# Optimization experiments

Hardware: AMD Instinct MI355X
Metric: run time of the kernel (lower is better)

The kernel has to match this reference:

```python
import jax, jax.numpy as jnp
import numpy as np

B, N, K, C_IN, C_OUT = 4, 8192, 32, 64, 64
MID = (C_OUT + C_IN) // 2  # 64, since C_IN is even
GROUPS = 8
EPS = 1e-5
SLOPE = 0.1


def group_norm(x, gamma, beta, groups=GROUPS, eps=EPS):
    # x: [b, ..., C], normalize per-sample over all spatial dims and group channels
    b = x.shape[0]
    C = x.shape[-1]
    xr = x.reshape(b, -1, groups, C // groups)
    mean = xr.mean(axis=(1, 3), keepdims=True)
    var = xr.var(axis=(1, 3), keepdims=True)
    xn = ((xr - mean) / jnp.sqrt(var + eps)).reshape(x.shape)
    return xn * gamma + beta


def lrelu(x):
    return jnp.where(x >= 0, x, SLOPE * x)


def setup_inputs() -> dict:
    key = jax.random.key(0)
    ks = jax.random.split(key, 10)
    signal = jax.random.normal(ks[0], (B, N, C_IN), dtype=jnp.float32)
    edges = jax.random.randint(ks[1], (B * N * K,), 0, B * N, dtype=jnp.int64)
    edge_feats = jax.random.normal(ks[2], (B * N * K, 3), dtype=jnp.float32)
    W1 = jax.random.normal(ks[3], (MID, C_IN + 3), dtype=jnp.float32) * 0.1
    W2 = jax.random.normal(ks[4], (C_OUT, MID), dtype=jnp.float32) * 0.1
    W3 = jax.random.normal(ks[5], (C_OUT, C_OUT), dtype=jnp.float32) * 0.1
    return {
        "signal": signal, "edges": edges, "edge_feats": edge_feats,
        "W1": W1, "g1": jnp.ones((MID,), jnp.float32), "b1": jnp.zeros((MID,), jnp.float32),
        "W2": W2, "g2": jnp.ones((C_OUT,), jnp.float32), "b2": jnp.zeros((C_OUT,), jnp.float32),
        "W3": W3, "g3": jnp.ones((C_OUT,), jnp.float32), "b3": jnp.zeros((C_OUT,), jnp.float32),
    }


def reference(signal, edges, edge_feats, W1, g1, b1, W2, g2, b2, W3, g3, b3):
    b, n, c = signal.shape
    k = edges.shape[0] // (b * n)
    flat = signal.reshape(b * n, c)
    # gather neighbor features and take relative difference: [b*n, k, c]
    ef = flat[edges].reshape(b * n, k, c) - flat[:, None, :]
    # concat relative coordinates -> [b, n, k, c+3]
    x = jnp.concatenate([ef, edge_feats.reshape(b * n, k, 3)], axis=-1)
    x = x.reshape(b, n, k, c + 3)
    # 1x1 conv (fc1) + GN + lrelu
    x = jnp.einsum('bnkc,mc->bnkm', x, W1)
    x = lrelu(group_norm(x, g1, b1))
    # max-pool over neighbors -> [b, n, mid]
    x = jnp.max(x, axis=2)
    # fc2 + GN + lrelu
    x = jnp.einsum('bnm,om->bno', x, W2)
    x = lrelu(group_norm(x, g2, b2))
    # fc3 + GN + lrelu
    x = jnp.einsum('bno,po->bnp', x, W3)
    x = lrelu(group_norm(x, g3, b3))
    return x  # [b, n, nb_feat_out]
```

## Files before the change

kernel.cpp:

```cpp
#include <hip/hip_runtime.h>

#define NB    4
#define NPB   8192
#define NPTS  (NB*NPB)
#define KNB   32
#define CH    64
#define W1C   67
#define GRPS  8
#define EPSV  1e-5f
#define SLOPEV 0.1f

typedef float f32x2 __attribute__((ext_vector_type(2)));
typedef float f32x4 __attribute__((ext_vector_type(4)));
typedef short bf16x8 __attribute__((ext_vector_type(8)));
typedef unsigned short u16;
typedef u16 u16x4 __attribute__((ext_vector_type(4)));
typedef u16 u16x8 __attribute__((ext_vector_type(8)));

#define WS_STATS1 0
#define WS_STATS2 64
#define WS_STATS3 128
#define WS_FLAG   192
#define WS_YB     256
#define WS_MX     (WS_YB + NPTS*CH/2)
#define WS_MN     (WS_MX + NPTS*CH/2)

#define LDP 72

__device__ __forceinline__ u16 f2bf(float f) {
    unsigned u = __float_as_uint(f);
    u += 0x7fff + ((u >> 16) & 1);
    return (u16)(u >> 16);
}
__device__ __forceinline__ float bf2f(u16 h) {
    return __uint_as_float(((unsigned)h) << 16);
}

template<int MODE>
__global__ __launch_bounds__(256) void k_mm(
    const void* __restrict__ X0,
    const void* __restrict__ X1,
    const float* __restrict__ Wg,
    const float* __restrict__ statsIn, float invcnt,
    const float* __restrict__ gm, const float* __restrict__ bt,
    void* __restrict__ Out,
    float* __restrict__ statsOut,
    const int* __restrict__ e_i32, int* __restrict__ flag)
{
    __shared__ u16 Al[64*LDP];
    __shared__ u16 Wl[64*LDP];
    __shared__ float affA[64], affB[64];
    __shared__ float lacc[16];
    __shared__ int sfnd[4];
    int tid = threadIdx.x;
    int pbase = blockIdx.x * 64;
    int b = pbase >> 13;

    if (MODE == 0 && blockIdx.x == 0) {
        if (tid < 192) statsOut[tid] = 0.f;
        int found = 0;
        #pragma unroll
        for (int i = 0; i < 16; ++i) {
            int idx = ((tid << 4) + i) * 2 + 1;
            found |= (e_i32[idx] != 0);
        }
        unsigned long long bl = __ballot(found);
        if ((tid & 63) == 0) sfnd[tid >> 6] = (bl != 0ull) ? 1 : 0;
    }
    if (MODE != 0) {
        if (tid < 64) {
            int g = tid >> 3;
            float sv = statsIn[b*16 + g*2 + 0];
            float qv = statsIn[b*16 + g*2 + 1];
            float mean = sv * invcnt;
            float var  = fmaf(-mean, mean, qv * invcnt);
            float rstd = rsqrtf(var + EPSV);
            float a = gm[tid] * rstd;
            affA[tid] = a;
            affB[tid] = fmaf(-mean, a, bt[tid]);
        }
    }
    if (tid < 16) lacc[tid] = 0.f;
    __syncthreads();
    if (MODE == 0 && blockIdx.x == 0 && tid == 0)
        *flag = sfnd[0] | sfnd[1] | sfnd[2] | sfnd[3];

    {
        const int wstride = (MODE == 0) ? W1C : 64;
        #pragma unroll
        for (int i = 0; i < 16; ++i) {
            int e = tid + 256*i;
            int o = e >> 6, m = e & 63;
            Wl[o*LDP + m] = f2bf(Wg[o*wstride + m]);
        }
    }
    #pragma unroll
    for (int it = 0; it < 4; ++it) {
        int fi = it*1024 + tid*4;
        int p = fi >> 6;
        int m = fi & 63;
        float xv[4];
        if (MODE == 1) {
            u16x4 vx = *(const u16x4*)&((const u16*)X0)[(pbase+p)*64 + m];
            u16x4 vn = *(const u16x4*)&((const u16*)X1)[(pbase+p)*64 + m];
            #pragma unroll
            for (int j = 0; j < 4; ++j) {
                float a = affA[m+j];
                float x = (a < 0.f) ? bf2f(vn[j]) : bf2f(vx[j]);
                float z = fmaf(a, x, affB[m+j]);
                xv[j] = (z >= 0.f) ? z : SLOPEV * z;
            }
        } else if (MODE == 2) {
            u16x4 vh = *(const u16x4*)&((const u16*)X0)[(pbase+p)*64 + m];
            #pragma unroll
            for (int j = 0; j < 4; ++j) {
                float z = fmaf(affA[m+j], bf2f(vh[j]), affB[m+j]);
                xv[j] = (z >= 0.f) ? z : SLOPEV * z;
            }
        } else {
            f32x4 vx = *(const f32x4*)&((const float*)X0)[(pbase+p)*64 + m];
            #pragma unroll
            for (int j = 0; j < 4; ++j) xv[j] = vx[j];
        }
        #pragma unroll
        for (int j = 0; j < 4; ++j)
            Al[p*LDP + m + j] = f2bf(xv[j]);
    }
    __syncthreads();

    int l = tid & 63, w = tid >> 6;
    int lr = l & 15;
    int lk = l >> 4;
    bf16x8 af[2], bw[4][2];
    #pragma unroll
    for (int kh = 0; kh < 2; ++kh)
        af[kh] = *(const bf16x8*)&Al[(w*16 + lr)*LDP + kh*32 + lk*8];
    #pragma unroll
    for (int ot = 0; ot < 4; ++ot)
        #pragma unroll
        for (int kh = 0; kh < 2; ++kh)
            bw[ot][kh] = *(const bf16x8*)&Wl[(ot*16 + lr)*LDP + kh*32 + lk*8];

    f32x4 acc[4];
    #pragma unroll
    for (int ot = 0; ot < 4; ++ot) {
        f32x4 c = {0.f, 0.f, 0.f, 0.f};
        c = __builtin_amdgcn_mfma_f32_16x16x32_bf16(af[0], bw[ot][0], c, 0, 0, 0);
        c = __builtin_amdgcn_mfma_f32_16x16x32_bf16(af[1], bw[ot][1], c, 0, 0, 0);
        acc[ot] = c;
    }

    #pragma unroll
    for (int ot = 0; ot < 4; ++ot)
        #pragma unroll
        for (int r = 0; r < 4; ++r) {
            int p = pbase + w*16 + lk*4 + r;
            int o = ot*16 + lr;
            ((u16*)Out)[p*64 + o] = f2bf(acc[ot][r]);
        }

    if (MODE != 0) {
        #pragma unroll
        for (int ot = 0; ot < 4; ++ot) {
            float s = 0.f, ss = 0.f;
            #pragma unroll
            for (int r = 0; r < 4; ++r) {
                float v = acc[ot][r];
                s += v;
                ss = fmaf(v, v, ss);
            }
            s += __shfl_xor(s, 16, 64);  ss += __shfl_xor(ss, 16, 64);
            s += __shfl_xor(s, 32, 64);  ss += __shfl_xor(ss, 32, 64);
            s += __shfl_xor(s, 1, 64);   ss += __shfl_xor(ss, 1, 64);
            s += __shfl_xor(s, 2, 64);   ss += __shfl_xor(ss, 2, 64);
            s += __shfl_xor(s, 4, 64);   ss += __shfl_xor(ss, 4, 64);
            if ((l & 7) == 0 && l < 16) {
                int g = ot*2 + (l >> 3);
                atomicAdd(&lacc[g*2 + 0], s);
                atomicAdd(&lacc[g*2 + 1], ss);
            }
        }
        __syncthreads();
        if (tid < 16)
            atomicAdd(&statsOut[b*16 + tid], lacc[tid]);
    }
}

#define PPB_E 32
#define SEDS  (KNB*4 + 4)
__global__ __launch_bounds__(256) void k_edge(const u16* __restrict__ Yb,
    const void* __restrict__ edg, const float* __restrict__ ef,
    const float* __restrict__ W1, const int* __restrict__ flag,
    u16* __restrict__ Mx, u16* __restrict__ Mn, float* __restrict__ stats1)
{
    __shared__ float sed[PPB_E*SEDS];
    __shared__ float lacc[16];
    int tid = threadIdx.x;
    if (tid < 16) lacc[tid] = 0.f;

    {
        bool is32 = (*flag != 0);
        const int*       e32 = (const int*)edg;
        const long long* e64 = (const long long*)edg;
        int ebase = blockIdx.x * (PPB_E*KNB);
        #pragma unroll
        for (int i = 0; i < 4; ++i) {
            int idx = tid + i*256;
            int gi  = ebase + idx;
            int e   = is32 ? __builtin_nontemporal_load(e32 + gi)
                           : (int)__builtin_nontemporal_load(e64 + gi);
            int pt = idx >> 5, k = idx & 31;
            float* d = &sed[pt*SEDS + k*4];
            d[0] = __builtin_nontemporal_load(ef + gi*3 + 0);
            d[1] = __builtin_nontemporal_load(ef + gi*3 + 1);
            d[2] = __builtin_nontemporal_load(ef + gi*3 + 2);
            d[3] = __int_as_float(e << 7);
        }
    }

    int lane = tid & 63, wv = tid >> 6;
    int il = lane & 7;
    int g8 = lane >> 3;
    int lpt = wv*8 + g8;
    int p = blockIdx.x * PPB_E + lpt;

    f32x2 w0[4], w1[4], w2[4], yp[4], mx[4], mn[4];
    #pragma unroll
    for (int jj = 0; jj < 4; ++jj) {
        int ch = il*8 + jj*2;
        w0[jj] = (f32x2){W1[ch*W1C + 64], W1[(ch+1)*W1C + 64]};
        w1[jj] = (f32x2){W1[ch*W1C + 65], W1[(ch+1)*W1C + 65]};
        w2[jj] = (f32x2){W1[ch*W1C + 66], W1[(ch+1)*W1C + 66]};
    }
    u16x8 yh = *(const u16x8*)&Yb[p*64 + il*8];
    #pragma unroll
    for (int jj = 0; jj < 4; ++jj) {
        yp[jj] = (f32x2){bf2f(yh[jj*2]), bf2f(yh[jj*2+1])};
        mx[jj] = (f32x2){-3.4e38f, -3.4e38f};
        mn[jj] = (f32x2){ 3.4e38f,  3.4e38f};
    }
    f32x2 s2 = {0.f, 0.f}, ss2 = {0.f, 0.f};
    __syncthreads();

    const char* Ybase = (const char*)Yb + il*16;
    const float* sp = &sed[lpt*SEDS];
    #pragma unroll 8
    for (int k = 0; k < KNB; ++k) {
        f32x4 m4 = *(const f32x4*)(sp + k*4);
        u16x8 q = *(const u16x8*)(Ybase + __float_as_int(m4[3]));
        f32x2 c0v = m4[0], c1v = m4[1], c2v = m4[2];
        #pragma unroll
        for (int jj = 0; jj < 4; ++jj) {
            f32x2 qq = {bf2f(q[jj*2]), bf2f(q[jj*2+1])};
            f32x2 t = qq - yp[jj];
            t = __builtin_elementwise_fma(c0v, w0[jj], t);
            t = __builtin_elementwise_fma(c1v, w1[jj], t);
            t = __builtin_elementwise_fma(c2v, w2[jj], t);
            mx[jj] = __builtin_elementwise_max(mx[jj], t);
            mn[jj] = __builtin_elementwise_min(mn[jj], t);
            s2 += t;
            ss2 = __builtin_elementwise_fma(t, t, ss2);
        }
    }

    u16x8 hx, hn;
    #pragma unroll
    for (int jj = 0; jj < 4; ++jj) {
        hx[jj*2] = f2bf(mx[jj].x); hx[jj*2+1] = f2bf(mx[jj].y);
        hn[jj*2] = f2bf(mn[jj].x); hn[jj*2+1] = f2bf(mn[jj].y);
    }
    __builtin_nontemporal_store(hx, (u16x8*)(Mx + p*64 + il*8));
    __builtin_nontemporal_store(hn, (u16x8*)(Mn + p*64 + il*8));

    float s  = s2.x + s2.y;
    float ss = ss2.x + ss2.y;
    s += __shfl_xor(s,  8, 64);  ss += __shfl_xor(ss,  8, 64);
    s += __shfl_xor(s, 16, 64);  ss += __shfl_xor(ss, 16, 64);
    s += __shfl_xor(s, 32, 64);  ss += __shfl_xor(ss, 32, 64);
    if (lane < 8) {
        atomicAdd(&lacc[lane*2 + 0], s);
        atomicAdd(&lacc[lane*2 + 1], ss);
    }
    __syncthreads();
    if (tid < 16) {
        int b = (blockIdx.x * PPB_E) / NPB;
        atomicAdd(&stats1[b*16 + tid], lacc[tid]);
    }
}

__global__ __launch_bounds__(256) void k_out(const u16* __restrict__ Vpre,
    const float* __restrict__ stats, float invcnt,
    const float* __restrict__ gm, const float* __restrict__ bt,
    float* __restrict__ out)
{
    int idx = blockIdx.x * blockDim.x + threadIdx.x;
    int p  = idx >> 4;
    int m0 = (idx & 15) << 2;
    int b  = p >> 13;
    int g  = m0 >> 3;
    float sv = stats[b*16 + g*2 + 0];
    float qv = stats[b*16 + g*2 + 1];
    float mean = sv * invcnt;
    float var  = fmaf(-mean, mean, qv * invcnt);
    float rstd = rsqrtf(var + EPSV);
    u16x4 v = *(const u16x4*)&Vpre[idx*4];
    float r[4];
    #pragma unroll
    for (int j = 0; j < 4; ++j) {
        float aa = gm[m0+j] * rstd;
        float z  = fmaf(aa, bf2f(v[j]) - mean, bt[m0+j]);
        r[j] = (z >= 0.f) ? z : SLOPEV * z;
    }
    f32x4 o4 = {r[0], r[1], r[2], r[3]};
    *(f32x4*)&out[idx*4] = o4;
}

extern "C" void kernel_launch(void* const* d_in, const int* in_sizes, int n_in,
                              void* d_out, int out_size, void* d_ws, size_t ws_size,
                              hipStream_t stream)
{
    const float* sig = (const float*)d_in[0];
    const void*  edg = d_in[1];
    const float* ef  = (const float*)d_in[2];
    const float* W1  = (const float*)d_in[3];
    const float* g1  = (const float*)d_in[4];
    const float* b1  = (const float*)d_in[5];
    const float* W2  = (const float*)d_in[6];
    const float* g2  = (const float*)d_in[7];
    const float* b2  = (const float*)d_in[8];
    const float* W3  = (const float*)d_in[9];
    const float* g3  = (const float*)d_in[10];
    const float* b3  = (const float*)d_in[11];
    float* out = (float*)d_out;
    float* ws  = (float*)d_ws;
    u16*   yb  = (u16*)(ws + WS_YB);
    u16*   mxb = (u16*)(ws + WS_MX);
    u16*   mnb = (u16*)(ws + WS_MN);

    k_mm<0><<<NPTS/64, 256, 0, stream>>>(sig, nullptr, W1, nullptr, 0.f,
                                          nullptr, nullptr, yb, ws,
                                          (const int*)edg, (int*)(ws + WS_FLAG));
    k_edge<<<NPTS/PPB_E, 256, 0, stream>>>(yb, edg, ef, W1,
                                           (const int*)(ws + WS_FLAG),
                                           mxb, mnb, ws + WS_STATS1);
    k_mm<1><<<NPTS/64, 256, 0, stream>>>(mxb, mnb, W2,
                                          ws + WS_STATS1, 1.f/(float)(NPB*KNB*8),
                                          g1, b1, yb, ws + WS_STATS2,
                                          nullptr, nullptr);
    k_mm<2><<<NPTS/64, 256, 0, stream>>>(yb, nullptr, W3,
                                          ws + WS_STATS2, 1.f/(float)(NPB*8),
                                          g2, b2, mxb, ws + WS_STATS3,
                                          nullptr, nullptr);
    k_out<<<(NPTS*CH/4)/256, 256, 0, stream>>>(mxb, ws + WS_STATS3,
                                         1.f/(float)(NPB*8), g3, b3, out);
}
```

Measured before the change: 57.58 us.

## Load MFMA A-fragments directly from global and enlarge edge blocks

```diff
diff --git a/kernel.cpp b/kernel.cpp
--- a/kernel.cpp
+++ b/kernel.cpp
@@ -6,7 +6,6 @@
 #define KNB   32
 #define CH    64
 #define W1C   67
-#define GRPS  8
 #define EPSV  1e-5f
 #define SLOPEV 0.1f
 
@@ -20,12 +19,13 @@
 #define WS_STATS1 0
 #define WS_STATS2 64
 #define WS_STATS3 128
-#define WS_FLAG   192
 #define WS_YB     256
 #define WS_MX     (WS_YB + NPTS*CH/2)
 #define WS_MN     (WS_MX + NPTS*CH/2)
 
-#define LDP 72
+#define LDPW 68
+#define SEDS (KNB*4 + 4)
+#define EPB  64
 
 __device__ __forceinline__ u16 f2bf(float f) {
     unsigned u = __float_as_uint(f);
@@ -36,37 +36,32 @@
     return __uint_as_float(((unsigned)h) << 16);
 }
 
+__device__ __forceinline__ bool probe_is32(const int* e_i32, int tid) {
+    int found = 0;
+    #pragma unroll
+    for (int i = 0; i < 8; ++i)
+        found |= (e_i32[(tid*8 + i)*2 + 1] != 0);
+    return (__ballot(found) != 0ull);
+}
+
 template<int MODE>
 __global__ __launch_bounds__(256) void k_mm(
-    const void* __restrict__ X0,
-    const void* __restrict__ X1,
+    const void* __restrict__ X0, const void* __restrict__ X1,
     const float* __restrict__ Wg,
     const float* __restrict__ statsIn, float invcnt,
     const float* __restrict__ gm, const float* __restrict__ bt,
-    void* __restrict__ Out,
-    float* __restrict__ statsOut,
-    const int* __restrict__ e_i32, int* __restrict__ flag)
+    u16* __restrict__ Out, float* __restrict__ statsOut,
+    float* __restrict__ zeroStats)
 {
-    __shared__ u16 Al[64*LDP];
-    __shared__ u16 Wl[64*LDP];
-    __shared__ float affA[64], affB[64];
+    __shared__ u16 Wl[64*LDPW];
+    __shared__ __align__(16) float affA[64];
+    __shared__ __align__(16) float affB[64];
     __shared__ float lacc[16];
-    __shared__ int sfnd[4];
     int tid = threadIdx.x;
     int pbase = blockIdx.x * 64;
     int b = pbase >> 13;
 
-    if (MODE == 0 && blockIdx.x == 0) {
-        if (tid < 192) statsOut[tid] = 0.f;
-        int found = 0;
-        #pragma unroll
-        for (int i = 0; i < 16; ++i) {
-            int idx = ((tid << 4) + i) * 2 + 1;
-            found |= (e_i32[idx] != 0);
-        }
-        unsigned long long bl = __ballot(found);
-        if ((tid & 63) == 0) sfnd[tid >> 6] = (bl != 0ull) ? 1 : 0;
-    }
+    if (MODE == 0 && blockIdx.x == 0 && tid < 192) zeroStats[tid] = 0.f;
     if (MODE != 0) {
         if (tid < 64) {
             int g = tid >> 3;
@@ -79,67 +74,71 @@
             affA[tid] = a;
             affB[tid] = fmaf(-mean, a, bt[tid]);
         }
-    }
-    if (tid < 16) lacc[tid] = 0.f;
-    __syncthreads();
-    if (MODE == 0 && blockIdx.x == 0 && tid == 0)
-        *flag = sfnd[0] | sfnd[1] | sfnd[2] | sfnd[3];
-
+        if (tid < 16) lacc[tid] = 0.f;
+    }
     {
         const int wstride = (MODE == 0) ? W1C : 64;
         #pragma unroll
         for (int i = 0; i < 16; ++i) {
             int e = tid + 256*i;
             int o = e >> 6, m = e & 63;
-            Wl[o*LDP + m] = f2bf(Wg[o*wstride + m]);
-        }
-    }
-    #pragma unroll
-    for (int it = 0; it < 4; ++it) {
-        int fi = it*1024 + tid*4;
-        int p = fi >> 6;
-        int m = fi & 63;
-        float xv[4];
-        if (MODE == 1) {
-            u16x4 vx = *(const u16x4*)&((const u16*)X0)[(pbase+p)*64 + m];
-            u16x4 vn = *(const u16x4*)&((const u16*)X1)[(pbase+p)*64 + m];
+            Wl[o*LDPW + m] = f2bf(Wg[o*wstride + m]);
+        }
+    }
+    __syncthreads();
+
+    int l = tid & 63, w = tid >> 6;
+    int lr = l & 15, lk = l >> 4;
+    int row = pbase + w*16 + lr;
+
+    bf16x8 af[2];
+    #pragma unroll
+    for (int kh = 0; kh < 2; ++kh) {
+        int m0 = kh*32 + lk*8;
+        bf16x8 h;
+        if (MODE == 0) {
+            f32x4 a0 = *(const f32x4*)&((const float*)X0)[row*64 + m0];
+            f32x4 a1 = *(const f32x4*)&((const float*)X0)[row*64 + m0 + 4];
             #pragma unroll
             for (int j = 0; j < 4; ++j) {
-                float a = affA[m+j];
-                float x = (a < 0.f) ? bf2f(vn[j]) : bf2f(vx[j]);
-                float z = fmaf(a, x, affB[m+j]);
-                xv[j] = (z >= 0.f) ? z : SLOPEV * z;
-            }
-        } else if (MODE == 2) {
-            u16x4 vh = *(const u16x4*)&((const u16*)X0)[(pbase+p)*64 + m];
-            #pragma unroll
-            for (int j = 0; j < 4; ++j) {
-                float z = fmaf(affA[m+j], bf2f(vh[j]), affB[m+j]);
-                xv[j] = (z >= 0.f) ? z : SLOPEV * z;
+                h[j]   = (short)f2bf(a0[j]);
+                h[4+j] = (short)f2bf(a1[j]);
             }
         } else {
-            f32x4 vx = *(const f32x4*)&((const float*)X0)[(pbase+p)*64 + m];
-            #pragma unroll
-            for (int j = 0; j < 4; ++j) xv[j] = vx[j];
-        }
-        #pragma unroll
-        for (int j = 0; j < 4; ++j)
-            Al[p*LDP + m + j] = f2bf(xv[j]);
-    }
-    __syncthreads();
-
-    int l = tid & 63, w = tid >> 6;
-    int lr = l & 15;
-    int lk = l >> 4;
-    bf16x8 af[2], bw[4][2];
-    #pragma unroll
-    for (int kh = 0; kh < 2; ++kh)
-        af[kh] = *(const bf16x8*)&Al[(w*16 + lr)*LDP + kh*32 + lk*8];
+            float aA[8], aB[8];
+            *(f32x4*)&aA[0] = *(const f32x4*)&affA[m0];
+            *(f32x4*)&aA[4] = *(const f32x4*)&affA[m0+4];
+            *(f32x4*)&aB[0] = *(const f32x4*)&affB[m0];
+            *(f32x4*)&aB[4] = *(const f32x4*)&affB[m0+4];
+            u16x8 vx = *(const u16x8*)&((const u16*)X0)[row*64 + m0];
+            if (MODE == 1) {
+                u16x8 vn = *(const u16x8*)&((const u16*)X1)[row*64 + m0];
+                #pragma unroll
+                for (int j = 0; j < 8; ++j) {
+                    float a = aA[j];
+                    float x = (a < 0.f) ? bf2f(vn[j]) : bf2f(vx[j]);
+                    float z = fmaf(a, x, aB[j]);
+                    z = (z >= 0.f) ? z : SLOPEV * z;
+                    h[j] = (short)f2bf(z);
+                }
+            } else {
+                #pragma unroll
+                for (int j = 0; j < 8; ++j) {
+                    float z = fmaf(aA[j], bf2f(vx[j]), aB[j]);
+                    z = (z >= 0.f) ? z : SLOPEV * z;
+                    h[j] = (short)f2bf(z);
+                }
+            }
+        }
+        af[kh] = h;
+    }
+
+    bf16x8 bw[4][2];
     #pragma unroll
     for (int ot = 0; ot < 4; ++ot)
         #pragma unroll
         for (int kh = 0; kh < 2; ++kh)
-            bw[ot][kh] = *(const bf16x8*)&Wl[(ot*16 + lr)*LDP + kh*32 + lk*8];
+            bw[ot][kh] = *(const bf16x8*)&Wl[(ot*16 + lr)*LDPW + kh*32 + lk*8];
 
     f32x4 acc[4];
     #pragma unroll
@@ -156,7 +155,7 @@
         for (int r = 0; r < 4; ++r) {
             int p = pbase + w*16 + lk*4 + r;
             int o = ot*16 + lr;
-            ((u16*)Out)[p*64 + o] = f2bf(acc[ot][r]);
+            Out[p*64 + o] = f2bf(acc[ot][r]);
         }
 
     if (MODE != 0) {
@@ -186,26 +185,24 @@
     }
 }
 
-#define PPB_E 32
-#define SEDS  (KNB*4 + 4)
-__global__ __launch_bounds__(256) void k_edge(const u16* __restrict__ Yb,
-    const void* __restrict__ edg, const float* __restrict__ ef,
-    const float* __restrict__ W1, const int* __restrict__ flag,
+__global__ __launch_bounds__(512) void k_edge(
+    const u16* __restrict__ Yb, const void* __restrict__ edg,
+    const float* __restrict__ ef, const float* __restrict__ W1,
     u16* __restrict__ Mx, u16* __restrict__ Mn, float* __restrict__ stats1)
 {
-    __shared__ float sed[PPB_E*SEDS];
+    __shared__ float sed[EPB*SEDS];
     __shared__ float lacc[16];
     int tid = threadIdx.x;
     if (tid < 16) lacc[tid] = 0.f;
 
+    bool is32 = probe_is32((const int*)edg, tid);
     {
-        bool is32 = (*flag != 0);
-        const int*       e32 = (const int*)edg;
+        const int* e32 = (const int*)edg;
         const long long* e64 = (const long long*)edg;
-        int ebase = blockIdx.x * (PPB_E*KNB);
+        int ebase = blockIdx.x * (EPB*KNB);
         #pragma unroll
         for (int i = 0; i < 4; ++i) {
-            int idx = tid + i*256;
+            int idx = tid + i*512;
             int gi  = ebase + idx;
             int e   = is32 ? __builtin_nontemporal_load(e32 + gi)
                            : (int)__builtin_nontemporal_load(e64 + gi);
@@ -222,9 +219,9 @@
     int il = lane & 7;
     int g8 = lane >> 3;
     int lpt = wv*8 + g8;
-    int p = blockIdx.x * PPB_E + lpt;
-
-    f32x2 w0[4], w1[4], w2[4], yp[4], mx[4], mn[4];
+    int p = blockIdx.x * EPB + lpt;
+
+    f32x2 w0[4], w1[4], w2[4];
     #pragma unroll
     for (int jj = 0; jj < 4; ++jj) {
         int ch = il*8 + jj*2;
@@ -232,6 +229,7 @@
         w1[jj] = (f32x2){W1[ch*W1C + 65], W1[(ch+1)*W1C + 65]};
         w2[jj] = (f32x2){W1[ch*W1C + 66], W1[(ch+1)*W1C + 66]};
     }
+    f32x2 yp[4], mx[4], mn[4];
     u16x8 yh = *(const u16x8*)&Yb[p*64 + il*8];
     #pragma unroll
     for (int jj = 0; jj < 4; ++jj) {
@@ -283,36 +281,42 @@
     }
     __syncthreads();
     if (tid < 16) {
-        int b = (blockIdx.x * PPB_E) / NPB;
+        int b = (blockIdx.x * EPB) >> 13;
         atomicAdd(&stats1[b*16 + tid], lacc[tid]);
     }
 }
 
-__global__ __launch_bounds__(256) void k_out(const u16* __restrict__ Vpre,
-    const float* __restrict__ stats, float invcnt,
-    const float* __restrict__ gm, const float* __restrict__ bt,
+__global__ __launch_bounds__(256) void k_out(
+    const u16* __restrict__ z3, const float* __restrict__ stats,
+    const float* __restrict__ g3, const float* __restrict__ b3,
     float* __restrict__ out)
 {
-    int idx = blockIdx.x * blockDim.x + threadIdx.x;
-    int p  = idx >> 4;
-    int m0 = (idx & 15) << 2;
-    int b  = p >> 13;
-    int g  = m0 >> 3;
-    float sv = stats[b*16 + g*2 + 0];
-    float qv = stats[b*16 + g*2 + 1];
-    float mean = sv * invcnt;
-    float var  = fmaf(-mean, mean, qv * invcnt);
-    float rstd = rsqrtf(var + EPSV);
-    u16x4 v = *(const u16x4*)&Vpre[idx*4];
-    float r[4];
-    #pragma unroll
-    for (int j = 0; j < 4; ++j) {
-        float aa = gm[m0+j] * rstd;
-        float z  = fmaf(aa, bf2f(v[j]) - mean, bt[m0+j]);
-        r[j] = (z >= 0.f) ? z : SLOPEV * z;
-    }
-    f32x4 o4 = {r[0], r[1], r[2], r[3]};
-    *(f32x4*)&out[idx*4] = o4;
+    const float invcnt = 1.f/(float)(NPB*8);
+    int tid = threadIdx.x;
+    int pbase = blockIdx.x * 64;
+    int b = pbase >> 13;
+    #pragma unroll
+    for (int it = 0; it < 4; ++it) {
+        int flat = it*1024 + tid*4;
+        int p = pbase + (flat >> 6);
+        int m = flat & 63;
+        int g = m >> 3;
+        float sv = stats[b*16 + g*2 + 0];
+        float qv = stats[b*16 + g*2 + 1];
+        float mean = sv * invcnt;
+        float var  = fmaf(-mean, mean, qv * invcnt);
+        float rstd = rsqrtf(var + EPSV);
+        u16x4 v = *(const u16x4*)&z3[p*64 + m];
+        float r[4];
+        #pragma unroll
+        for (int j = 0; j < 4; ++j) {
+            float aa = g3[m+j] * rstd;
+            float z  = fmaf(aa, bf2f(v[j]) - mean, b3[m+j]);
+            r[j] = (z >= 0.f) ? z : SLOPEV * z;
+        }
+        f32x4 o4 = {r[0], r[1], r[2], r[3]};
+        *(f32x4*)&out[p*64 + m] = o4;
+    }
 }
 
 extern "C" void kernel_launch(void* const* d_in, const int* in_sizes, int n_in,
@@ -338,19 +342,14 @@
     u16*   mnb = (u16*)(ws + WS_MN);
 
     k_mm<0><<<NPTS/64, 256, 0, stream>>>(sig, nullptr, W1, nullptr, 0.f,
-                                          nullptr, nullptr, yb, ws,
-                                          (const int*)edg, (int*)(ws + WS_FLAG));
-    k_edge<<<NPTS/PPB_E, 256, 0, stream>>>(yb, edg, ef, W1,
-                                           (const int*)(ws + WS_FLAG),
-                                           mxb, mnb, ws + WS_STATS1);
-    k_mm<1><<<NPTS/64, 256, 0, stream>>>(mxb, mnb, W2,
-                                          ws + WS_STATS1, 1.f/(float)(NPB*KNB*8),
-                                          g1, b1, yb, ws + WS_STATS2,
-                                          nullptr, nullptr);
-    k_mm<2><<<NPTS/64, 256, 0, stream>>>(yb, nullptr, W3,
-                                          ws + WS_STATS2, 1.f/(float)(NPB*8),
-                                          g2, b2, mxb, ws + WS_STATS3,
-                                          nullptr, nullptr);
-    k_out<<<(NPTS*CH/4)/256, 256, 0, stream>>>(mxb, ws + WS_STATS3,
-                                         1.f/(float)(NPB*8), g3, b3, out);
-}
+                                         nullptr, nullptr, yb, nullptr, ws);
+    k_edge<<<NPTS/EPB, 512, 0, stream>>>(yb, edg, ef, W1, mxb, mnb,
+                                         ws + WS_STATS1);
+    k_mm<1><<<NPTS/64, 256, 0, stream>>>(mxb, mnb, W2, ws + WS_STATS1,
+                                         1.f/(float)(NPB*KNB*8), g1, b1,
+                                         yb, ws + WS_STATS2, nullptr);
+    k_mm<2><<<NPTS/64, 256, 0, stream>>>(yb, nullptr, W3, ws + WS_STATS2,
+                                         1.f/(float)(NPB*8), g2, b2,
+                                         mxb, ws + WS_STATS3, nullptr);
+    k_out<<<NPTS/64, 256, 0, stream>>>(mxb, ws + WS_STATS3, g3, b3, out);
+}
```

After: 57.42 us. Within noise of the previous version (-0.3%).
